# Kernel optimization log

Measured on AMD Instinct MI355X. Metric: run time of the kernel, lower is better.

Reference implementation:

```python
import jax, jax.numpy as jnp
import numpy as np

BINS = 50            # init kwarg
SCALING = (-1.0, 1.0)  # init kwarg
EPS = 1e-6


def setup_inputs() -> dict:
    key = jax.random.key(0)
    X = jax.random.normal(key, (256, 6, 128), dtype=jnp.float32)
    return {"X": X}


def reference(X) -> jnp.ndarray:
    lo, hi = SCALING
    W = X.shape[-1]
    lead = X.shape[:-1]

    # --- minmax_scaler: scale last dim into [lo, hi] ---
    X_min = X.min(axis=-1, keepdims=True)
    X_max = X.max(axis=-1, keepdims=True)
    X_scaled = (X - X_min) / (X_max - X_min + EPS) * (hi - lo) + lo

    # --- bucketize: torch.bucketize(right=False) == searchsorted side='left' ---
    boundaries = jnp.linspace(lo, hi, BINS + 1)[1:-1]  # (bins-1,) inner edges
    n_bins = boundaries.shape[0] + 1                   # == BINS
    binned = jnp.searchsorted(boundaries, X_scaled, side='left')  # int, same shape as X

    bflat = binned.reshape(-1, W)      # (S, W), S = prod(lead)
    S = bflat.shape[0]

    # --- mtm_compute: per-series transition histogram via scatter-add ---
    idx = bflat[:, :-1] * n_bins + bflat[:, 1:]        # (S, W-1) flat (i->j) indices
    mtm = jnp.zeros((S, n_bins * n_bins), dtype=X.dtype)
    mtm = mtm.at[jnp.arange(S)[:, None], idx].add(jnp.ones_like(idx, dtype=X.dtype))
    mtm = mtm.reshape(S, n_bins, n_bins)
    row_sum = mtm.sum(axis=-1, keepdims=True)          # (S, n_bins, 1)
    mtm = mtm / jnp.where(row_sum == 0, 1.0, row_sum)  # row-normalize, guard empty rows

    # --- final gather: MTF[t1, t2] = mtm[bin(t1), bin(t2)] ---
    mtm_flat = mtm.reshape(S, n_bins * n_bins)
    gidx = (n_bins * bflat[:, :, None] + bflat[:, None, :]).reshape(S, W * W)
    mtf = jnp.take_along_axis(mtm_flat, gidx, axis=1)  # (S, W*W)
    return mtf.reshape(lead + (W, W))
```

## Files before the change

kernel.cpp:

```cpp
#include <hip/hip_runtime.h>
#include <float.h>

#define W  128
#define NB 50

__global__ __launch_bounds__(256) void mtf_kernel(const float* __restrict__ X,
                                                  float* __restrict__ out) {
    __shared__ int   bins[W];
    __shared__ int   hist[NB * NB];
    __shared__ int   rowsum[NB];
    __shared__ float probs[NB * NB];
    __shared__ float redmin[4], redmax[4];

    const int tid = threadIdx.x;
    const int s   = blockIdx.x;
    const float* xrow = X + (size_t)s * W;

    float v = 0.0f;
    float vmin = FLT_MAX, vmax = -FLT_MAX;
    if (tid < W) { v = xrow[tid]; vmin = v; vmax = v; }
    #pragma unroll
    for (int off = 32; off >= 1; off >>= 1) {
        vmin = fminf(vmin, __shfl_down(vmin, off, 64));
        vmax = fmaxf(vmax, __shfl_down(vmax, off, 64));
    }
    if ((tid & 63) == 0) { redmin[tid >> 6] = vmin; redmax[tid >> 6] = vmax; }

    for (int i = tid; i < NB * NB; i += 256) hist[i] = 0;
    if (tid < NB) rowsum[tid] = 0;
    __syncthreads();

    const float mn = fminf(fminf(redmin[0], redmin[1]), fminf(redmin[2], redmin[3]));
    const float mx = fmaxf(fmaxf(redmax[0], redmax[1]), fmaxf(redmax[2], redmax[3]));
    const float d  = (mx - mn) + 1e-6f;

    if (tid < W) {
        float q   = (v - mn) / d;
        float xsc = q * 2.0f - 1.0f;
        double xd = (double)xsc;
        int b = 0;
        #pragma unroll
        for (int k = 1; k <= NB - 1; ++k) {
            double bk = -1.0 + 0.04 * (double)k;
            b += (bk < xd) ? 1 : 0;
        }
        bins[tid] = b;
    }
    __syncthreads();

    if (tid < W - 1) {
        int bi = bins[tid], bj = bins[tid + 1];
        atomicAdd(&hist[bi * NB + bj], 1);
        atomicAdd(&rowsum[bi], 1);
    }
    __syncthreads();

    for (int i = tid; i < NB * NB; i += 256) {
        int rs = rowsum[i / NB];
        probs[i] = (float)hist[i] / (float)(rs == 0 ? 1 : rs);
    }
    __syncthreads();

    float* orow = out + (size_t)s * W * W;
    const int c4 = (tid & 31) * 4;
    const int r0 = tid >> 5;
    const int b0 = bins[c4], b1 = bins[c4 + 1], b2 = bins[c4 + 2], b3 = bins[c4 + 3];
    #pragma unroll
    for (int it = 0; it < 16; ++it) {
        int row = r0 + it * 8;
        int rb  = bins[row] * NB;
        float4 o;
        o.x = probs[rb + b0];
        o.y = probs[rb + b1];
        o.z = probs[rb + b2];
        o.w = probs[rb + b3];
        *(float4*)(orow + row * W + c4) = o;
    }
}

extern "C" void kernel_launch(void* const* d_in, const int* in_sizes, int n_in,
                              void* d_out, int out_size, void* d_ws, size_t ws_size,
                              hipStream_t stream) {
    const float* X = (const float*)d_in[0];
    float* out = (float*)d_out;
    int S = in_sizes[0] / W;
    mtf_kernel<<<dim3(S), dim3(256), 0, stream>>>(X, out);
}
```

Measured before the change: 104.9 us.

## Pre-gather probability columns per half-tile and stream rows with nontemporal stores

Replaces the normalized 50x50 probability table with a 50x64 table already indexed by column bins, built separately for each half of the output columns. Each output float4 then comes from a single vectorized LDS read instead of four scattered scalar reads. Output writes use nontemporal stores to avoid polluting the cache. This adds an extra sync and a second table build per block, and makes each row-of-bins lookup per thread register-held.

```diff
diff --git a/kernel.cpp b/kernel.cpp
--- a/kernel.cpp
+++ b/kernel.cpp
@@ -1,15 +1,18 @@
 #include <hip/hip_runtime.h>
 #include <float.h>
 
-#define W  128
-#define NB 50
+#define W   128
+#define NB  50
+#define GC  64
+
+typedef float f32x4 __attribute__((ext_vector_type(4)));
 
 __global__ __launch_bounds__(256) void mtf_kernel(const float* __restrict__ X,
                                                   float* __restrict__ out) {
     __shared__ int   bins[W];
     __shared__ int   hist[NB * NB];
     __shared__ int   rowsum[NB];
-    __shared__ float probs[NB * NB];
+    __shared__ float G[NB][GC];
     __shared__ float redmin[4], redmax[4];
 
     const int tid = threadIdx.x;
@@ -48,6 +51,12 @@
     }
     __syncthreads();
 
+    const int r0 = tid >> 4;
+    const int cc = (tid & 15) * 4;
+    int rbrow[8];
+    #pragma unroll
+    for (int it = 0; it < 8; ++it) rbrow[it] = bins[r0 + it * 16];
+
     if (tid < W - 1) {
         int bi = bins[tid], bj = bins[tid + 1];
         atomicAdd(&hist[bi * NB + bj], 1);
@@ -55,26 +64,28 @@
     }
     __syncthreads();
 
-    for (int i = tid; i < NB * NB; i += 256) {
-        int rs = rowsum[i / NB];
-        probs[i] = (float)hist[i] / (float)(rs == 0 ? 1 : rs);
-    }
-    __syncthreads();
+    float* orow = out + (size_t)s * W * W;
 
-    float* orow = out + (size_t)s * W * W;
-    const int c4 = (tid & 31) * 4;
-    const int r0 = tid >> 5;
-    const int b0 = bins[c4], b1 = bins[c4 + 1], b2 = bins[c4 + 2], b3 = bins[c4 + 3];
     #pragma unroll
-    for (int it = 0; it < 16; ++it) {
-        int row = r0 + it * 8;
-        int rb  = bins[row] * NB;
-        float4 o;
-        o.x = probs[rb + b0];
-        o.y = probs[rb + b1];
-        o.z = probs[rb + b2];
-        o.w = probs[rb + b3];
-        *(float4*)(orow + row * W + c4) = o;
+    for (int p = 0; p < 2; ++p) {
+        const int C0 = p * GC;
+
+        for (int i = tid; i < NB * GC; i += 256) {
+            int b  = i >> 6;
+            int c  = i & (GC - 1);
+            int rs = rowsum[b];
+            G[b][c] = (float)hist[b * NB + bins[C0 + c]]
+                    / (float)(rs == 0 ? 1 : rs);
+        }
+        __syncthreads();
+
+        #pragma unroll
+        for (int it = 0; it < 8; ++it) {
+            int r = r0 + it * 16;
+            f32x4 o = *(const f32x4*)&G[rbrow[it]][cc];
+            __builtin_nontemporal_store(o, (f32x4*)(orow + r * W + C0 + cc));
+        }
+        if (p == 0) __syncthreads();
     }
 }
 
```

New measurement: 110.2 us. 5.1% more time.
